# Kernel optimization log

Hardware: AMD Instinct MI355X
Metric: run time of the kernel (lower is better)

Reference implementation:

```python
import jax, jax.numpy as jnp
import numpy as np

BETA = 0.99
EPS = 1e-05


def setup_inputs() -> dict:
    key = jax.random.key(0)
    s = jax.random.normal(key, (16, 2000, 257, 2), dtype=jnp.float32)
    return {"s": s}


def reference(s):
    # s: (N, T, F, C). Unbiased EWMA mean/var normalization, sequential over T.
    N, T, F, C = s.shape
    st = jnp.transpose(s, (1, 0, 2, 3))  # (T, N, F, C) for scan over time
    zeros = jnp.zeros((N, F, C), dtype=s.dtype)
    one = jnp.asarray(1.0, dtype=s.dtype)
    beta = jnp.asarray(BETA, dtype=s.dtype)

    def step(carry, x):
        beta_t, v1, v2, S = carry
        beta_t = beta * beta_t
        v1 = beta * v1 + (1 - beta) * x
        v2_prev = v2
        v2 = v1 / (1 - beta_t)
        w = (1 - beta) / (1 - beta_t)
        S = (1 - w) * S + w * (x - v2) * (x - v2_prev)
        S = S * (S > 0)  # clamp negative variance to 0 (as in original)
        y = (x - v2) / jnp.sqrt(S + EPS)
        return (beta_t, v1, v2, S), y

    init = (one, zeros, zeros, zeros)
    _, out = jax.lax.scan(step, init, st)
    return jnp.transpose(out, (1, 0, 2, 3))  # back to (N, T, F, C)
```

## Files before the change

kernel.cpp:

```cpp
#include <hip/hip_runtime.h>


#define NN 16
#define TT 2000
#define FCC 514
#define SERIES (NN * FCC)
#define BETAF 0.99f
#define OMBF 0.01f
#define EPSF 1e-5f
#define NCHUNK 7
#define CLEN 286
#define WARM 512
#define PF 16

__device__ __constant__ const float BP[PF + 1] = {
    1.0f,
    0.99f,
    0.9801f,
    0.970299f,
    0.96059601f,
    0.9509900499f,
    0.941480149401f,
    0.93206534790699f,
    0.9227446944279201f,
    0.9134272474836409f,
    0.9042929750088045f,
    0.8952500452587165f,
    0.8862975448061293f,
    0.877434569357868f,
    0.8686602236642894f,
    0.8599736214276465f,
    0.8513738852133700f
};

__global__ __launch_bounds__(64) __attribute__((amdgpu_waves_per_eu(1, 1)))
void ewma_kernel(const float* __restrict__ s, float* __restrict__ out) {
    const int tid = blockIdx.x * 64 + threadIdx.x;
    if (tid >= SERIES) return;

    const int chunk = blockIdx.y;
    const int t_out = chunk * CLEN;
    int t_end = t_out + CLEN; if (t_end > TT) t_end = TT;
    int t0 = t_out - WARM;     if (t0 < 0) t0 = 0;

    const int n  = tid / FCC;
    const int fc = tid - n * FCC;

    double bd = 0.99, acc = 0.99;
    int e = t0;
    while (e) { if (e & 1) acc *= bd; bd *= bd; e >>= 1; }
    float btg = (float)acc;

    float v1 = 0.0f, v2p = 0.0f, S = 0.0f;

    const size_t base = (size_t)n * TT * FCC + (size_t)fc + (size_t)t0 * FCC;
    const float* p  = s   + base;
    float*       po = out + base;

    float buf[PF];
    #pragma unroll
    for (int i = 0; i < PF; ++i) buf[i] = p[i * FCC];

    int t = t0;
    while (t + PF <= t_end) {
        const float* pf_ptr = (t + 2 * PF <= t_end) ? (p + PF * FCC) : p;
        float nbuf[PF];
        #pragma unroll
        for (int i = 0; i < PF; ++i) {
            asm volatile("global_load_dword %0, %1, off"
                         : "=v"(nbuf[i])
                         : "v"(pf_ptr + i * FCC));
        }
        __builtin_amdgcn_sched_barrier(0);

        float rr[PF], ww[PF];
        #pragma unroll
        for (int i = 0; i < PF; ++i) {
            const float bt = btg * BP[i];
            const float om = 1.0f - bt;
            const float r  = __builtin_amdgcn_rcpf(om);
            rr[i] = r;
            ww[i] = OMBF * r;
        }
        btg *= BP[PF];

        #pragma unroll
        for (int i = 0; i < PF; ++i) {
            const float x  = buf[i];
            v1 = fmaf(BETAF, v1, OMBF * x);
            const float v2 = v1 * rr[i];
            const float d  = x - v2;
            const float dp = x - v2p;
            const float pr = d * dp;
            S = fmaf(ww[i], pr - S, S);
            S = fmaxf(S, 0.0f);
            const float y = d * __builtin_amdgcn_rsqf(S + EPSF);
            v2p = v2;
            if (t >= t_out) {
                __builtin_nontemporal_store(y, po + i * FCC);
            } else if (t + i >= t_out) {
                __builtin_nontemporal_store(y, po + i * FCC);
            }
        }

        asm volatile("s_waitcnt vmcnt(0)" ::: "memory");
        __builtin_amdgcn_sched_barrier(0);
        #pragma unroll
        for (int i = 0; i < PF; ++i) buf[i] = nbuf[i];

        p  += PF * FCC;
        po += PF * FCC;
        t  += PF;
    }
    for (; t < t_end; ++t) {
        const float x  = *p;
        const float om = 1.0f - btg;
        const float r  = __builtin_amdgcn_rcpf(om);
        const float w  = OMBF * r;
        btg *= BETAF;
        v1 = fmaf(BETAF, v1, OMBF * x);
        const float v2 = v1 * r;
        const float d  = x - v2;
        const float dp = x - v2p;
        const float pr = d * dp;
        S = fmaf(w, pr - S, S);
        S = fmaxf(S, 0.0f);
        const float y = d * __builtin_amdgcn_rsqf(S + EPSF);
        v2p = v2;
        if (t >= t_out) __builtin_nontemporal_store(y, po);
        p  += FCC;
        po += FCC;
    }
}

extern "C" void kernel_launch(void* const* d_in, const int* in_sizes, int n_in,
                              void* d_out, int out_size, void* d_ws, size_t ws_size,
                              hipStream_t stream) {
    const float* s = (const float*)d_in[0];
    float* out = (float*)d_out;
    dim3 grid((SERIES + 63) / 64, NCHUNK);
    ewma_kernel<<<grid, dim3(64), 0, stream>>>(s, out);
}
```

Measured before the change: 151.3 us.

## Stream inputs through double-buffered LDS via global_load_lds and defer output stores

Input prefetch now goes through global_load_lds into a two-slot LDS ring of 16 timesteps per slot, which keeps two blocks of loads in flight instead of one register buffer. Outputs for each block are held in registers and stored at the start of the next iteration, so the stores overlap the next block's compute. Nontemporal stores become plain stores, and the waves_per_eu attribute is replaced by launch_bounds(64,1). The vmcnt-based waits assume global_load_lds and the stores share the same counter, so store ordering may add stalls or correctness risk.

```diff
diff --git a/kernel.cpp b/kernel.cpp
--- a/kernel.cpp
+++ b/kernel.cpp
@@ -33,9 +33,18 @@
     0.8513738852133700f
 };
 
-__global__ __launch_bounds__(64) __attribute__((amdgpu_waves_per_eu(1, 1)))
+__device__ __forceinline__ void ld_lds(const float* g, float* l) {
+    __builtin_amdgcn_global_load_lds(
+        (const __attribute__((address_space(1))) void*)g,
+        (__attribute__((address_space(3))) void*)l, 4, 0, 0);
+}
+
+__global__ __launch_bounds__(64, 1)
 void ewma_kernel(const float* __restrict__ s, float* __restrict__ out) {
-    const int tid = blockIdx.x * 64 + threadIdx.x;
+    __shared__ float lds[2][PF][64];
+
+    const int lane = threadIdx.x;
+    const int tid  = blockIdx.x * 64 + lane;
     if (tid >= SERIES) return;
 
     const int chunk = blockIdx.y;
@@ -57,77 +66,91 @@
     const float* p  = s   + base;
     float*       po = out + base;
 
-    float buf[PF];
+    __attribute__((address_space(3))) float* l3 =
+        (__attribute__((address_space(3))) float*)&lds[0][0][lane];
+    const unsigned lbase = (unsigned)(uintptr_t)l3;
+
     #pragma unroll
-    for (int i = 0; i < PF; ++i) buf[i] = p[i * FCC];
+    for (int i = 0; i < PF; ++i) ld_lds(p + i * FCC,        &lds[0][i][0]);
+    #pragma unroll
+    for (int i = 0; i < PF; ++i) ld_lds(p + (PF + i) * FCC, &lds[1][i][0]);
+    asm volatile("s_waitcnt vmcnt(16)" ::: "memory");
+    __builtin_amdgcn_sched_barrier(0);
+
+    float yprev[PF];
+    #pragma unroll
+    for (int i = 0; i < PF; ++i) yprev[i] = 0.0f;
 
     int t = t0;
+    int par = 0;
     while (t + PF <= t_end) {
-        const float* pf_ptr = (t + 2 * PF <= t_end) ? (p + PF * FCC) : p;
-        float nbuf[PF];
+        #pragma unroll
+        for (int i = 0; i < PF; ++i)
+            if (t - PF + i >= t_out) po[(i - PF) * FCC] = yprev[i];
+
+        float x[PF];
+        const unsigned abase = lbase + (unsigned)par * (PF * 256);
+        #pragma unroll
+        for (int i = 0; i < PF; ++i)
+            asm volatile("ds_read_b32 %0, %1"
+                         : "=v"(x[i]) : "v"(abase + (unsigned)(i * 256)));
+        asm volatile("s_waitcnt lgkmcnt(0)" ::: "memory");
+        __builtin_amdgcn_sched_barrier(0);
+
+        {
+            const float* gsrc = (t + 3 * PF <= t_end) ? (p + 2 * PF * FCC) : p;
+            #pragma unroll
+            for (int i = 0; i < PF; ++i) ld_lds(gsrc + i * FCC, &lds[par][i][0]);
+        }
+
+        float rr[PF];
+        #pragma unroll
+        for (int i = 0; i < PF; ++i)
+            rr[i] = __builtin_amdgcn_rcpf(1.0f - btg * BP[i]);
+        btg *= BP[PF];
         #pragma unroll
         for (int i = 0; i < PF; ++i) {
-            asm volatile("global_load_dword %0, %1, off"
-                         : "=v"(nbuf[i])
-                         : "v"(pf_ptr + i * FCC));
+            const float xx = x[i];
+            const float r  = rr[i];
+            const float w  = OMBF * r;
+            v1 = fmaf(BETAF, v1, OMBF * xx);
+            const float v2 = v1 * r;
+            const float d  = xx - v2;
+            const float dp = xx - v2p;
+            S = fmaf(w, d * dp - S, S);
+            S = fmaxf(S, 0.0f);
+            yprev[i] = d * __builtin_amdgcn_rsqf(S + EPSF);
+            v2p = v2;
         }
+
+        asm volatile("s_waitcnt vmcnt(16)" ::: "memory");
         __builtin_amdgcn_sched_barrier(0);
 
-        float rr[PF], ww[PF];
-        #pragma unroll
-        for (int i = 0; i < PF; ++i) {
-            const float bt = btg * BP[i];
-            const float om = 1.0f - bt;
-            const float r  = __builtin_amdgcn_rcpf(om);
-            rr[i] = r;
-            ww[i] = OMBF * r;
-        }
-        btg *= BP[PF];
+        par ^= 1;
+        p += PF * FCC; po += PF * FCC; t += PF;
+    }
 
-        #pragma unroll
-        for (int i = 0; i < PF; ++i) {
-            const float x  = buf[i];
-            v1 = fmaf(BETAF, v1, OMBF * x);
-            const float v2 = v1 * rr[i];
-            const float d  = x - v2;
-            const float dp = x - v2p;
-            const float pr = d * dp;
-            S = fmaf(ww[i], pr - S, S);
-            S = fmaxf(S, 0.0f);
-            const float y = d * __builtin_amdgcn_rsqf(S + EPSF);
-            v2p = v2;
-            if (t >= t_out) {
-                __builtin_nontemporal_store(y, po + i * FCC);
-            } else if (t + i >= t_out) {
-                __builtin_nontemporal_store(y, po + i * FCC);
-            }
-        }
+    #pragma unroll
+    for (int i = 0; i < PF; ++i)
+        if (t - PF + i >= t_out) po[(i - PF) * FCC] = yprev[i];
 
-        asm volatile("s_waitcnt vmcnt(0)" ::: "memory");
-        __builtin_amdgcn_sched_barrier(0);
-        #pragma unroll
-        for (int i = 0; i < PF; ++i) buf[i] = nbuf[i];
+    asm volatile("s_waitcnt vmcnt(0)" ::: "memory");
+    __builtin_amdgcn_sched_barrier(0);
 
-        p  += PF * FCC;
-        po += PF * FCC;
-        t  += PF;
-    }
     for (; t < t_end; ++t) {
-        const float x  = *p;
-        const float om = 1.0f - btg;
-        const float r  = __builtin_amdgcn_rcpf(om);
+        const float xx = *p;
+        const float r  = __builtin_amdgcn_rcpf(1.0f - btg);
         const float w  = OMBF * r;
         btg *= BETAF;
-        v1 = fmaf(BETAF, v1, OMBF * x);
+        v1 = fmaf(BETAF, v1, OMBF * xx);
         const float v2 = v1 * r;
-        const float d  = x - v2;
-        const float dp = x - v2p;
-        const float pr = d * dp;
-        S = fmaf(w, pr - S, S);
+        const float d  = xx - v2;
+        const float dp = xx - v2p;
+        S = fmaf(w, d * dp - S, S);
         S = fmaxf(S, 0.0f);
         const float y = d * __builtin_amdgcn_rsqf(S + EPSF);
         v2p = v2;
-        if (t >= t_out) __builtin_nontemporal_store(y, po);
+        if (t >= t_out) *po = y;
         p  += FCC;
         po += FCC;
     }
```

Result: faster. 144.7 us (-4.4%).
